# Kernel tuning notes

Hardware: AMD Instinct MI355X
Metric: run time of the kernel (lower is better)

Reference implementation:

```python
import jax, jax.numpy as jnp
import numpy as np

A, B, D, H = 64, 256, 128, 512  # seq rows, columns (encoder batch / decode loop), n_dims, hidden


def _lstm_step(Wih, Whh, bih, bhh, h, c, x):
    # x: [N, D], h/c: [N, H]; PyTorch gate order i, f, g, o
    gates = x @ Wih.T + bih + h @ Whh.T + bhh  # [N, 4H]
    i, f, g, o = jnp.split(gates, 4, axis=-1)
    c = jax.nn.sigmoid(f) * c + jax.nn.sigmoid(i) * jnp.tanh(g)
    h = jax.nn.sigmoid(o) * jnp.tanh(c)
    return h, c


def setup_inputs() -> dict:
    key = jax.random.key(0)
    ks = jax.random.split(key, 12)
    s = 0.05
    inp = {
        "input_tensor": jax.random.normal(ks[0], (A, B, D), jnp.float32),
        "enc_Wih": jax.random.normal(ks[1], (4 * H, D), jnp.float32) * s,
        "enc_Whh": jax.random.normal(ks[2], (4 * H, H), jnp.float32) * s,
        "enc_bih": jax.random.normal(ks[3], (4 * H,), jnp.float32) * s,
        "enc_bhh": jax.random.normal(ks[4], (4 * H,), jnp.float32) * s,
        "dec_Wih": jax.random.normal(ks[5], (4 * H, D), jnp.float32) * s,
        "dec_Whh": jax.random.normal(ks[6], (4 * H, H), jnp.float32) * s,
        "dec_bih": jax.random.normal(ks[7], (4 * H,), jnp.float32) * s,
        "dec_bhh": jax.random.normal(ks[8], (4 * H,), jnp.float32) * s,
        "lin_W": jax.random.normal(ks[9], (D, H), jnp.float32) * s,
        "lin_b": jax.random.normal(ks[10], (D,), jnp.float32) * s,
    }
    return inp


def reference(input_tensor, enc_Wih, enc_Whh, enc_bih, enc_bhh,
              dec_Wih, dec_Whh, dec_bih, dec_bhh, lin_W, lin_b):
    a, b, d = input_tensor.shape
    h_dim = enc_Whh.shape[1]
    dt = input_tensor.dtype

    # ---- encoder: seq-first LSTM over dim0 (len a), batch = b ----
    def e_step(hc, x_t):
        h, c = hc
        h, c = _lstm_step(enc_Wih, enc_Whh, enc_bih, enc_bhh, h, c, x_t)
        return (h, c), None

    h0 = jnp.zeros((b, h_dim), dt)
    (hN, cN), _ = jax.lax.scan(e_step, (h0, h0), input_tensor)
    # hidden[0][:, -1].unsqueeze(1): keep only the LAST batch element -> [1, H]
    dh, dc = hN[-1:], cN[-1:]

    # ---- decoder: loop i = b-1 .. 0; emit linear(h) then run length-a LSTM on column i ----
    def col_step(hc, x_col):  # x_col: [a, d]
        h, c = hc
        out_i = (h @ lin_W.T + lin_b)[0]  # [d], emitted BEFORE processing the column

        def t_step(hc2, x_t):
            h2, c2 = hc2
            h2, c2 = _lstm_step(dec_Wih, dec_Whh, dec_bih, dec_bhh, h2, c2, x_t[None])
            return (h2, c2), None

        (h, c), _ = jax.lax.scan(t_step, (h, c), x_col)
        return (h, c), out_i

    x_cols = jnp.flip(jnp.transpose(input_tensor, (1, 0, 2)), 0)  # [b, a, d], reversed i
    _, outs = jax.lax.scan(col_step, (dh, dc), x_cols)  # [b, d] in reversed order
    outs = jnp.flip(outs, 0)
    # outputs[:, i, :] = [1, d] row broadcast across all a rows
    return jnp.broadcast_to(outs[None, :, :], (a, b, d))
```

## Files before the change

### kernel.cpp

```cpp
#include <hip/hip_runtime.h>
#include <math.h>

#define A_ 64
#define B_ 256
#define D_ 128
#define H_ 512
#define STEPS_ENC 64
#define STEPS_TOT (64 + 16384)
#define NWG 32
#define NTHREADS 1024

#define XCC_GETREG_IMM (20 | (31 << 11))

#define OFF_XT    0
#define N_XT      (A_*D_*B_)
#define OFF_HT0   (OFF_XT + N_XT)
#define OFF_HT1   (OFF_HT0 + H_*B_)
#define OFF_CT    (OFF_HT1 + H_*B_)
#define OFF_HTAP  (OFF_CT + H_*B_)
#define OFF_HB64  (OFF_HTAP + B_*H_)
#define OFF_CINIT (OFF_HB64 + 4*H_)
#define OFF_ELECT (OFF_CINIT + H_)

__device__ __forceinline__ float tanhfast(float x) {
  return 1.0f - 2.0f * __builtin_amdgcn_rcpf(__expf(2.0f * x) + 1.0f);
}

__device__ __forceinline__ unsigned long long load_nt(const unsigned long long* p) {
  unsigned long long v;
  asm volatile("global_load_dwordx2 %0, %1, off nt\n\ts_waitcnt vmcnt(0)"
               : "=&v"(v) : "v"(p));
  return v;
}
__device__ __forceinline__ unsigned long long load_inv(const unsigned long long* p) {
  unsigned long long v;
  asm volatile("buffer_inv sc0\n\t"
               "global_load_dwordx2 %0, %1, off nt\n\ts_waitcnt vmcnt(0)"
               : "=&v"(v) : "v"(p));
  return v;
}
__device__ __forceinline__ void store_nt(unsigned long long* p, unsigned long long v) {
  asm volatile("global_store_dwordx2 %0, %1, off nt" :: "v"(p), "v"(v));
}

template<int CTRL>
__device__ __forceinline__ float dpp_ror_add(float x) {
  int y = __builtin_amdgcn_update_dpp(0, __float_as_int(x), CTRL, 0xF, 0xF, false);
  return x + __int_as_float(y);
}
__device__ __forceinline__ float row_allsum16(float x) {
  x = dpp_ror_add<0x128>(x);
  x = dpp_ror_add<0x124>(x);
  x = dpp_ror_add<0x122>(x);
  x = dpp_ror_add<0x121>(x);
  return x;
}

#define HSP 36
#define HS_N (16 * HSP)

__global__ void init0(float* __restrict__ ws) {
  unsigned long long* HB = (unsigned long long*)(ws + OFF_HB64);
  int* EL = (int*)(ws + OFF_ELECT);
  int j = threadIdx.x;
  HB[H_ + j] = 0ull;
  HB[j]      = 0xFFFFFFFF00000000ull;
  if (j < 8) EL[j] = 0;
  if (j == 8) EL[8] = -1;
}

template<int PHASE>
__device__ __forceinline__ void lstm_phase(
    const float* __restrict__ in0,
    const float* __restrict__ Wih, const float* __restrict__ Whh,
    const float* __restrict__ bih, const float* __restrict__ bhh,
    unsigned long long* __restrict__ HB, float* __restrict__ HTAP,
    float* hstage,
    int w, int v, int l, float& c,
    float actA, float actB, float actC)
{
  const int g = l >> 4;
  const int j = l & 15;
  const int u = (w << 4) + v;
  const int R = (g << 9) + u;

  float4 wh[8];
#pragma unroll
  for (int k = 0; k < 8; ++k)
    wh[k] = *(const float4*)&Whh[R * H_ + (j << 5) + (k << 2)];
  float4 wx0 = *(const float4*)&Wih[R * D_ + (j << 3)];
  float4 wx1 = *(const float4*)&Wih[R * D_ + (j << 3) + 4];
  const float bias = (j == 0) ? (bih[R] + bhh[R]) : 0.f;

  const int pe = (v << 5) + (l & 31);

  const int s0 = (PHASE == 0) ? 0 : STEPS_ENC;
  const int s1 = (PHASE == 0) ? STEPS_ENC : STEPS_TOT;

  for (int s = s0; s < s1; ++s) {
    const float* xp;
    if (PHASE == 0) {
      xp = in0 + (s * B_ + 255) * D_;
    } else {
      const int sd = s - STEPS_ENC;
      xp = in0 + ((sd & 63) * B_ + (255 - (sd >> 6))) * D_;
    }
    float4 x0 = *(const float4*)(xp + (j << 3));
    float4 x1 = *(const float4*)(xp + (j << 3) + 4);

    unsigned long long* slot = &HB[(((s + 1) & 1) << 9) + pe];
    unsigned long long pk;
    int spins = 0;
    for (;;) {
      pk = ((++spins & 63) == 0) ? load_inv(slot) : load_nt(slot);
      if (__all((unsigned)(pk >> 32) == (unsigned)s)) break;
    }
    float* hbuf = hstage + (s & 1) * HS_N;
    if (l < 32) hbuf[(v * HSP) + (l & 31)] = __uint_as_float((unsigned)pk);

    float acc0 = bias
               + wx0.x * x0.x + wx0.y * x0.y + wx0.z * x0.z + wx0.w * x0.w
               + wx1.x * x1.x + wx1.y * x1.y + wx1.z * x1.z + wx1.w * x1.w;

    __syncthreads();

    const float4* hp = (const float4*)&hbuf[j * HSP];
    float acc1 = 0.f;
#pragma unroll
    for (int k = 0; k < 8; k += 2) {
      float4 h4a = hp[k];
      float4 h4b = hp[k + 1];
      acc0 += wh[k].x * h4a.x + wh[k].y * h4a.y
            + wh[k].z * h4a.z + wh[k].w * h4a.w;
      acc1 += wh[k + 1].x * h4b.x + wh[k + 1].y * h4b.y
            + wh[k + 1].z * h4b.z + wh[k + 1].w * h4b.w;
    }

    float a = row_allsum16(acc0 + acc1);
    a = fmaf(actA, __builtin_amdgcn_rcpf(__expf(actB * a) + 1.0f), actC);
    float ai = __shfl(a, 0);
    float af = __shfl(a, 16);
    float ag = __shfl(a, 32);
    float ao = __shfl(a, 48);
    c = af * c + ai * ag;
    float hn = ao * tanhfast(c);
    if (l == 0) {
      if ((s & 63) == 63) {
        int q = s >> 6;
        if (q < 256) HTAP[q * H_ + u] = hn;
      }
      unsigned long long opk =
          ((unsigned long long)(unsigned)(s + 1) << 32) | __float_as_uint(hn);
      store_nt(&HB[((s & 1) << 9) + u], opk);
    }
  }
}

__global__ __launch_bounds__(NTHREADS, 1) void fused(
    const float* __restrict__ in0,
    const float* __restrict__ eWih, const float* __restrict__ eWhh,
    const float* __restrict__ ebih, const float* __restrict__ ebhh,
    const float* __restrict__ dWih, const float* __restrict__ dWhh,
    const float* __restrict__ dbih, const float* __restrict__ dbhh,
    float* __restrict__ ws)
{
  unsigned long long* HB = (unsigned long long*)(ws + OFF_HB64);
  float* HTAP = ws + OFF_HTAP;

  __shared__ __align__(16) float hstage[2][HS_N];
  __shared__ int role;

  const int tid = threadIdx.x;

  if (tid == 0) {
    unsigned xcc = ((unsigned)__builtin_amdgcn_s_getreg(XCC_GETREG_IMM)) & 7u;
    int* EL = (int*)(ws + OFF_ELECT);
    int r = __hip_atomic_fetch_add(&EL[xcc], 1, __ATOMIC_RELAXED,
                                   __HIP_MEMORY_SCOPE_AGENT);
    int myrole = -1;
    if (r < NWG) {
      if (r == NWG - 1) {
        int exp = -1;
        __hip_atomic_compare_exchange_strong(&EL[8], &exp, (int)xcc,
            __ATOMIC_RELAXED, __ATOMIC_RELAXED, __HIP_MEMORY_SCOPE_AGENT);
      }
      int wx;
      do {
        wx = __hip_atomic_load(&EL[8], __ATOMIC_RELAXED, __HIP_MEMORY_SCOPE_AGENT);
        if (wx == -1) __builtin_amdgcn_s_sleep(2);
      } while (wx == -1);
      if (wx == (int)xcc) myrole = r;
    }
    role = myrole;
  }
  __syncthreads();
  if (role < 0) return;
  const int w = role;

  const int v = tid >> 6;
  const int l = tid & 63;

  const int gate = l >> 4;
  const float actA = (gate == 2) ? -2.0f :  1.0f;
  const float actB = (gate == 2) ?  2.0f : -1.0f;
  const float actC = (gate == 2) ?  1.0f :  0.0f;

  float c = 0.f;

  lstm_phase<0>(in0, eWih, eWhh, ebih, ebhh, HB, HTAP, &hstage[0][0],
                w, v, l, c, actA, actB, actC);
  lstm_phase<1>(in0, dWih, dWhh, dbih, dbhh, HB, HTAP, &hstage[0][0],
                w, v, l, c, actA, actB, actC);
}

__global__ __launch_bounds__(128) void out_proj(
    const float* __restrict__ ws, const float* __restrict__ linW,
    const float* __restrict__ linb, float* __restrict__ out) {
  const float* HTAP = ws + OFF_HTAP;
  __shared__ float hs[H_];
  const int b = blockIdx.x;
  const int i = 255 - b;
  const int d = threadIdx.x;
  *(float4*)&hs[4 * d] = *(const float4*)&HTAP[i * H_ + 4 * d];
  __syncthreads();
  float acc = linb[d];
#pragma unroll 8
  for (int k = 0; k < H_; k += 4) {
    float4 w4 = *(const float4*)&linW[d * H_ + k];
    acc += w4.x * hs[k] + w4.y * hs[k + 1] + w4.z * hs[k + 2] + w4.w * hs[k + 3];
  }
  for (int a = 0; a < A_; ++a)
    out[(a * B_ + b) * D_ + d] = acc;
}

extern "C" void kernel_launch(void* const* d_in, const int* in_sizes, int n_in,
                              void* d_out, int out_size, void* d_ws, size_t ws_size,
                              hipStream_t stream) {
  const float* in0  = (const float*)d_in[0];
  const float* eWih = (const float*)d_in[1];
  const float* eWhh = (const float*)d_in[2];
  const float* ebih = (const float*)d_in[3];
  const float* ebhh = (const float*)d_in[4];
  const float* dWih = (const float*)d_in[5];
  const float* dWhh = (const float*)d_in[6];
  const float* dbih = (const float*)d_in[7];
  const float* dbhh = (const float*)d_in[8];
  const float* linW = (const float*)d_in[9];
  const float* linb = (const float*)d_in[10];
  float* ws = (float*)d_ws;
  float* out = (float*)d_out;

  init0<<<1, 512, 0, stream>>>(ws);
  fused<<<256, NTHREADS, 0, stream>>>(in0, eWih, eWhh, ebih, ebhh,
                                      dWih, dWhh, dbih, dbhh, ws);
  out_proj<<<256, 128, 0, stream>>>(ws, linW, linb, out);
}
```

Before: 18.30 ms.

## Stage recurrent weights in LDS and give each lane all four gates

Moves the per-unit Whh slice out of registers into a 128KB dynamic LDS buffer. The work split changes from 16 lanes per gate to every lane computing partial dot products for all four gates over 8 hidden elements. Gate sums now use full 64-lane reductions (DPP, swizzle and shuffle), and activations are evaluated per gate without the per-lane select constants. The aims are fewer LDS h reads after the barrier and lower register pressure. In exchange each step adds LDS weight reads and four longer cross-lane reductions on the serial critical path.

```diff
diff --git a/kernel.cpp b/kernel.cpp
--- a/kernel.cpp
+++ b/kernel.cpp
@@ -9,6 +9,8 @@
 #define STEPS_TOT (64 + 16384)
 #define NWG 32
 #define NTHREADS 1024
+#define WHLDS_N 32768
+#define DYN_LDS ((WHLDS_N + 1024) * 4)
 
 #define XCC_GETREG_IMM (20 | (31 << 11))
 
@@ -22,6 +24,9 @@
 #define OFF_CINIT (OFF_HB64 + 4*H_)
 #define OFF_ELECT (OFF_CINIT + H_)
 
+__device__ __forceinline__ float sigf(float x) {
+  return __builtin_amdgcn_rcpf(1.0f + __expf(-x));
+}
 __device__ __forceinline__ float tanhfast(float x) {
   return 1.0f - 2.0f * __builtin_amdgcn_rcpf(__expf(2.0f * x) + 1.0f);
 }
@@ -44,20 +49,24 @@
 }
 
 template<int CTRL>
-__device__ __forceinline__ float dpp_ror_add(float x) {
+__device__ __forceinline__ float dpp_add(float x) {
   int y = __builtin_amdgcn_update_dpp(0, __float_as_int(x), CTRL, 0xF, 0xF, false);
   return x + __int_as_float(y);
 }
-__device__ __forceinline__ float row_allsum16(float x) {
-  x = dpp_ror_add<0x128>(x);
-  x = dpp_ror_add<0x124>(x);
-  x = dpp_ror_add<0x122>(x);
-  x = dpp_ror_add<0x121>(x);
+__device__ __forceinline__ float allsum64(float x, int l) {
+  x = dpp_add<0x128>(x);
+  x = dpp_add<0x124>(x);
+  x = dpp_add<0x122>(x);
+  x = dpp_add<0x121>(x);
+  int y = __builtin_amdgcn_ds_swizzle(__float_as_int(x), 0x401F);
+  x += __int_as_float(y);
+  x += __shfl(x, l ^ 32);
   return x;
 }
 
-#define HSP 36
-#define HS_N (16 * HSP)
+__device__ __forceinline__ float dot4(float4 a, float4 b) {
+  return a.x * b.x + a.y * b.y + a.z * b.z + a.w * b.w;
+}
 
 __global__ void init0(float* __restrict__ ws) {
   unsigned long long* HB = (unsigned long long*)(ws + OFF_HB64);
@@ -75,24 +84,32 @@
     const float* __restrict__ Wih, const float* __restrict__ Whh,
     const float* __restrict__ bih, const float* __restrict__ bhh,
     unsigned long long* __restrict__ HB, float* __restrict__ HTAP,
-    float* hstage,
-    int w, int v, int l, float& c,
-    float actA, float actB, float actC)
+    float* __restrict__ whlds,
+    float* __restrict__ hstage,
+    int w, int v, int l, float& c)
 {
-  const int g = l >> 4;
-  const int j = l & 15;
   const int u = (w << 4) + v;
-  const int R = (g << 9) + u;
-
-  float4 wh[8];
+
+  {
+    float* wb = whlds + (v << 11);
 #pragma unroll
-  for (int k = 0; k < 8; ++k)
-    wh[k] = *(const float4*)&Whh[R * H_ + (j << 5) + (k << 2)];
-  float4 wx0 = *(const float4*)&Wih[R * D_ + (j << 3)];
-  float4 wx1 = *(const float4*)&Wih[R * D_ + (j << 3) + 4];
-  const float bias = (j == 0) ? (bih[R] + bhh[R]) : 0.f;
+    for (int i = 0; i < 8; ++i) {
+      int fl = (l << 2) + (i << 8);
+      int gg = fl >> 9, kk = fl & 511;
+      *(float4*)&wb[fl] = *(const float4*)&Whh[((gg << 9) + u) * H_ + kk];
+    }
+  }
+  float2 wx0 = *(const float2*)&Wih[((0 << 9) + u) * D_ + (l << 1)];
+  float2 wx1 = *(const float2*)&Wih[((1 << 9) + u) * D_ + (l << 1)];
+  float2 wx2 = *(const float2*)&Wih[((2 << 9) + u) * D_ + (l << 1)];
+  float2 wx3 = *(const float2*)&Wih[((3 << 9) + u) * D_ + (l << 1)];
+  const float b0 = bih[(0 << 9) + u] + bhh[(0 << 9) + u];
+  const float b1 = bih[(1 << 9) + u] + bhh[(1 << 9) + u];
+  const float b2 = bih[(2 << 9) + u] + bhh[(2 << 9) + u];
+  const float b3 = bih[(3 << 9) + u] + bhh[(3 << 9) + u];
 
   const int pe = (v << 5) + (l & 31);
+  unsigned wboff = (unsigned)(v << 11);
 
   const int s0 = (PHASE == 0) ? 0 : STEPS_ENC;
   const int s1 = (PHASE == 0) ? STEPS_ENC : STEPS_TOT;
@@ -105,8 +122,7 @@
       const int sd = s - STEPS_ENC;
       xp = in0 + ((sd & 63) * B_ + (255 - (sd >> 6))) * D_;
     }
-    float4 x0 = *(const float4*)(xp + (j << 3));
-    float4 x1 = *(const float4*)(xp + (j << 3) + 4);
+    float2 xv = *(const float2*)(xp + (l << 1));
 
     unsigned long long* slot = &HB[(((s + 1) & 1) << 9) + pe];
     unsigned long long pk;
@@ -115,33 +131,46 @@
       pk = ((++spins & 63) == 0) ? load_inv(slot) : load_nt(slot);
       if (__all((unsigned)(pk >> 32) == (unsigned)s)) break;
     }
-    float* hbuf = hstage + (s & 1) * HS_N;
-    if (l < 32) hbuf[(v * HSP) + (l & 31)] = __uint_as_float((unsigned)pk);
-
-    float acc0 = bias
-               + wx0.x * x0.x + wx0.y * x0.y + wx0.z * x0.z + wx0.w * x0.w
-               + wx1.x * x1.x + wx1.y * x1.y + wx1.z * x1.z + wx1.w * x1.w;
+    float* hbuf = hstage + ((s & 1) << 9);
+    if (l < 32) hbuf[pe] = __uint_as_float((unsigned)pk);
+
+    asm volatile("" : "+v"(wboff));
+    const float* wb = whlds + wboff;
+
+    float a0 = wx0.x * xv.x + wx0.y * xv.y;
+    float a1 = wx1.x * xv.x + wx1.y * xv.y;
+    float a2 = wx2.x * xv.x + wx2.y * xv.y;
+    float a3 = wx3.x * xv.x + wx3.y * xv.y;
+
+    const int ko = l << 3;
+    float4 w0a = *(const float4*)&wb[(0 << 9) + ko];
+    float4 w0b = *(const float4*)&wb[(0 << 9) + ko + 4];
+    float4 w1a = *(const float4*)&wb[(1 << 9) + ko];
+    float4 w1b = *(const float4*)&wb[(1 << 9) + ko + 4];
+    float4 w2a = *(const float4*)&wb[(2 << 9) + ko];
+    float4 w2b = *(const float4*)&wb[(2 << 9) + ko + 4];
+    float4 w3a = *(const float4*)&wb[(3 << 9) + ko];
+    float4 w3b = *(const float4*)&wb[(3 << 9) + ko + 4];
 
     __syncthreads();
 
-    const float4* hp = (const float4*)&hbuf[j * HSP];
-    float acc1 = 0.f;
-#pragma unroll
-    for (int k = 0; k < 8; k += 2) {
-      float4 h4a = hp[k];
-      float4 h4b = hp[k + 1];
-      acc0 += wh[k].x * h4a.x + wh[k].y * h4a.y
-            + wh[k].z * h4a.z + wh[k].w * h4a.w;
-      acc1 += wh[k + 1].x * h4b.x + wh[k + 1].y * h4b.y
-            + wh[k + 1].z * h4b.z + wh[k + 1].w * h4b.w;
-    }
-
-    float a = row_allsum16(acc0 + acc1);
-    a = fmaf(actA, __builtin_amdgcn_rcpf(__expf(actB * a) + 1.0f), actC);
-    float ai = __shfl(a, 0);
-    float af = __shfl(a, 16);
-    float ag = __shfl(a, 32);
-    float ao = __shfl(a, 48);
+    float4 ha = *(const float4*)&hbuf[ko];
+    float4 hb = *(const float4*)&hbuf[ko + 4];
+
+    a0 += dot4(w0a, ha) + dot4(w0b, hb);
+    a1 += dot4(w1a, ha) + dot4(w1b, hb);
+    a2 += dot4(w2a, ha) + dot4(w2b, hb);
+    a3 += dot4(w3a, ha) + dot4(w3b, hb);
+
+    a0 = allsum64(a0, l) + b0;
+    a1 = allsum64(a1, l) + b1;
+    a2 = allsum64(a2, l) + b2;
+    a3 = allsum64(a3, l) + b3;
+
+    float ai = sigf(a0);
+    float af = sigf(a1);
+    float ag = tanhfast(a2);
+    float ao = sigf(a3);
     c = af * c + ai * ag;
     float hn = ao * tanhfast(c);
     if (l == 0) {
@@ -156,7 +185,7 @@
   }
 }
 
-__global__ __launch_bounds__(NTHREADS, 1) void fused(
+__global__ __launch_bounds__(NTHREADS) void fused(
     const float* __restrict__ in0,
     const float* __restrict__ eWih, const float* __restrict__ eWhh,
     const float* __restrict__ ebih, const float* __restrict__ ebhh,
@@ -167,7 +196,9 @@
   unsigned long long* HB = (unsigned long long*)(ws + OFF_HB64);
   float* HTAP = ws + OFF_HTAP;
 
-  __shared__ __align__(16) float hstage[2][HS_N];
+  extern __shared__ __align__(16) float smem[];
+  float* whlds  = smem;
+  float* hstage = smem + WHLDS_N;
   __shared__ int role;
 
   const int tid = threadIdx.x;
@@ -200,17 +231,12 @@
   const int v = tid >> 6;
   const int l = tid & 63;
 
-  const int gate = l >> 4;
-  const float actA = (gate == 2) ? -2.0f :  1.0f;
-  const float actB = (gate == 2) ?  2.0f : -1.0f;
-  const float actC = (gate == 2) ?  1.0f :  0.0f;
-
   float c = 0.f;
 
-  lstm_phase<0>(in0, eWih, eWhh, ebih, ebhh, HB, HTAP, &hstage[0][0],
-                w, v, l, c, actA, actB, actC);
-  lstm_phase<1>(in0, dWih, dWhh, dbih, dbhh, HB, HTAP, &hstage[0][0],
-                w, v, l, c, actA, actB, actC);
+  lstm_phase<0>(in0, eWih, eWhh, ebih, ebhh, HB, HTAP, whlds, hstage,
+                w, v, l, c);
+  lstm_phase<1>(in0, dWih, dWhh, dbih, dbhh, HB, HTAP, whlds, hstage,
+                w, v, l, c);
 }
 
 __global__ __launch_bounds__(128) void out_proj(
@@ -250,8 +276,11 @@
   float* ws = (float*)d_ws;
   float* out = (float*)d_out;
 
+  hipFuncSetAttribute((const void*)fused,
+                      hipFuncAttributeMaxDynamicSharedMemorySize, DYN_LDS);
+
   init0<<<1, 512, 0, stream>>>(ws);
-  fused<<<256, NTHREADS, 0, stream>>>(in0, eWih, eWhh, ebih, ebhh,
-                                      dWih, dWhh, dbih, dbhh, ws);
+  fused<<<256, NTHREADS, DYN_LDS, stream>>>(in0, eWih, eWhh, ebih, ebhh,
+                                            dWih, dWhh, dbih, dbhh, ws);
   out_proj<<<256, 128, 0, stream>>>(ws, linW, linb, out);
 }
```

Result: slower. 24.25 ms (+32.5%).
